# Performance work log

Measured on AMD Instinct MI355X. Metric: run time of the kernel, lower is better.

The kernel has to match this reference:

```python
import jax, jax.numpy as jnp
import numpy as np

N_NODES = 50000
N_EDGES = 1600000
D = 64


def setup_inputs() -> dict:
    key = jax.random.key(0)
    ks = jax.random.split(key, 7)
    scale = 1.0 / np.sqrt(2 * D)  # keep activations sane through relu stack
    x = jax.random.normal(ks[0], (N_NODES, D), dtype=jnp.float32)
    edge_index = jax.random.randint(ks[1], (2, N_EDGES), 0, N_NODES, dtype=jnp.int32)
    edge_weight = jax.random.uniform(ks[2], (N_EDGES,), dtype=jnp.float32)
    W1 = jax.random.normal(ks[3], (D, 2 * D), dtype=jnp.float32) * scale
    b1 = jax.random.normal(ks[4], (D,), dtype=jnp.float32) * 0.01
    W2 = jax.random.normal(ks[5], (D, 2 * D), dtype=jnp.float32) * scale
    b2 = jax.random.normal(ks[6], (D,), dtype=jnp.float32) * 0.01
    return {"x": x, "edge_index": edge_index, "edge_weight": edge_weight,
            "W1": W1, "b1": b1, "W2": W2, "b2": b2}


def _sage_conv(x, src, dst, edge_weight, W, b):
    # gather neighbor features, weight, scatter-mean onto src nodes
    m = x[dst] * edge_weight[:, None]                      # [E, d]
    agg_sum = jax.ops.segment_sum(m, src, num_segments=x.shape[0])
    cnt = jax.ops.segment_sum(jnp.ones_like(edge_weight), src,
                              num_segments=x.shape[0])
    agg = agg_sum / jnp.maximum(cnt, 1.0)[:, None]          # scatter 'mean'
    h = jnp.concatenate([x, agg], axis=1)                   # [N, 2d]
    return h @ W.T + b


def reference(x, edge_index, edge_weight, W1, b1, W2, b2):
    src, dst = edge_index[0], edge_index[1]
    h = jax.nn.relu(_sage_conv(x, src, dst, edge_weight, W1, b1))
    h = jax.nn.relu(_sage_conv(h, src, dst, edge_weight, W2, b2))
    return h
```

## Files before the change

kernel.cpp:

```cpp
#include <hip/hip_runtime.h>

#define NN 50000
#define NE 1600000
#define DD 64
#define NPB 196
#define NBKT 256
#define CHUNK 2500
#define NBLK 640
#define SLOT 24
#define S1CAP 1024
#define SPCAP 512
#define CSRCAP 8192

typedef __attribute__((ext_vector_type(8))) short bf16x8;
typedef __attribute__((ext_vector_type(4))) float f32x4;
typedef __attribute__((ext_vector_type(2))) float f32x2;

static __device__ __forceinline__ unsigned short f2bf(float f) {
    unsigned int u = __float_as_uint(f);
    unsigned int r = (u + 0x7FFFu + ((u >> 16) & 1u)) >> 16;
    return (unsigned short)r;
}
static __device__ __forceinline__ float bf2f(unsigned short h) {
    return __uint_as_float((unsigned int)h << 16);
}
static __device__ __forceinline__ unsigned int pk_fp8x4(float a, float b, float c, float d) {
    unsigned int p = __builtin_amdgcn_cvt_pk_fp8_f32(a, b, 0u, false);
    p = __builtin_amdgcn_cvt_pk_fp8_f32(c, d, p, true);
    return p;
}

__global__ __launch_bounds__(256) void prep(
    const float* __restrict__ x, ushort* __restrict__ xb,
    unsigned int* __restrict__ xf8,
    const float* __restrict__ W1, const float* __restrict__ W2,
    ushort* __restrict__ W1b, ushort* __restrict__ W2b,
    int* __restrict__ gcur)
{
    int b = blockIdx.x, tid = threadIdx.x;
    if (b < 3125) {
        int i = b * 256 + tid;
        float4 v = ((const float4*)x)[i];
        ushort4 o;
        o.x = f2bf(v.x); o.y = f2bf(v.y); o.z = f2bf(v.z); o.w = f2bf(v.w);
        ((ushort4*)xb)[i] = o;
        xf8[i] = pk_fp8x4(v.x, v.y, v.z, v.w);
    } else if (b < 3141) {
        int i = (b - 3125) * 256 + tid;
        const float* src = (i < 2048) ? W1 : W2;
        ushort* dst = (i < 2048) ? W1b : W2b;
        int j = i & 2047;
        float4 v = ((const float4*)src)[j];
        ushort4 o;
        o.x = f2bf(v.x); o.y = f2bf(v.y); o.z = f2bf(v.z); o.w = f2bf(v.w);
        ((ushort4*)dst)[j] = o;
    } else {
        for (int i = tid; i < 2304; i += 256) gcur[i] = 0;
    }
}

__global__ __launch_bounds__(256) void bin_lds(
    const int* __restrict__ ei, const float* __restrict__ ew,
    int* __restrict__ gcur, int* __restrict__ gspillc,
    int2* __restrict__ buf1, int2* __restrict__ spill)
{
    __shared__ int2 slot[NBKT * SLOT];
    __shared__ int  lcnt[NBKT];
    __shared__ int  lbase[NBKT];
    int tid = threadIdx.x;
    int shard = blockIdx.x & 7;

    for (int b = tid; b < NBKT; b += 256) lcnt[b] = 0;
    __syncthreads();

    int e0 = blockIdx.x * CHUNK;
    for (int i = tid; i < CHUNK; i += 256) {
        int e = e0 + i;
        int s = ei[e];
        int d = ei[NE + e];
        float w = ew[e];
        int bkt = s / NPB;
        int sloc = s - bkt * NPB;
        int2 rec = make_int2(d | ((int)f2bf(w) << 16), sloc);
        int pos = atomicAdd(&lcnt[bkt], 1);
        if (pos < SLOT) {
            slot[bkt * SLOT + pos] = rec;
        } else {
            int sp = atomicAdd(&gspillc[bkt], 1);
            if (sp < SPCAP) spill[bkt * SPCAP + sp] = rec;
        }
    }
    __syncthreads();

    {
        int b = tid;
        int n = lcnt[b]; if (n > SLOT) n = SLOT;
        lcnt[b] = n;
        lbase[b] = (n > 0) ? atomicAdd(&gcur[b * 8 + shard], n) : 0;
    }
    __syncthreads();

    int wave = tid >> 6, lane = tid & 63;
    int b0 = wave * 64;
    int vcnt = lcnt[b0 + lane];
    int vbase = lbase[b0 + lane];
#pragma unroll 8
    for (int j = 0; j < 64; ++j) {
        int n = __shfl(vcnt, j);
        int base = __shfl(vbase, j);
        int b = b0 + j;
        if (lane < n) {
            int2 rec = slot[b * SLOT + lane];
            int p = base + lane;
            if (p < S1CAP) {
                buf1[((size_t)b * 8 + shard) * S1CAP + p] = rec;
            } else {
                int sp = atomicAdd(&gspillc[b], 1);
                if (sp < SPCAP) spill[b * SPCAP + sp] = rec;
            }
        }
    }
}

__global__ __launch_bounds__(1024) void build_csr(
    const int* __restrict__ gcur, const int2* __restrict__ buf1,
    const int* __restrict__ gspillc, const int2* __restrict__ spill,
    unsigned int* __restrict__ csr, int* __restrict__ rstart,
    int* __restrict__ cnt)
{
    __shared__ int lcnt[NPB];
    __shared__ int lstart[NPB];
    __shared__ int sa[256], sb[256];
    int tid = threadIdx.x, bkt = blockIdx.x;

    if (tid < NPB) lcnt[tid] = 0;
    __syncthreads();

    for (int sh = 0; sh < 9; ++sh) {
        int n; const int2* rp;
        if (sh < 8) {
            n = gcur[bkt * 8 + sh]; if (n > S1CAP) n = S1CAP;
            rp = buf1 + ((size_t)bkt * 8 + sh) * S1CAP;
        } else {
            n = gspillc[bkt]; if (n > SPCAP) n = SPCAP;
            rp = spill + (size_t)bkt * SPCAP;
        }
        for (int i = tid; i < n; i += 1024)
            atomicAdd(&lcnt[rp[i].y], 1);
    }
    __syncthreads();

    if (tid < 256) sa[tid] = (tid < NPB) ? ((lcnt[tid] + 3) & ~3) : 0;
    __syncthreads();
    int* s = sa; int* d = sb;
    for (int off = 1; off < 256; off <<= 1) {
        if (tid < 256) d[tid] = s[tid] + (tid >= off ? s[tid - off] : 0);
        __syncthreads();
        int* t = s; s = d; d = t;
    }
    if (tid < NPB) {
        int ex = (tid == 0) ? 0 : s[tid - 1];
        lstart[tid] = ex;
        int node = bkt * NPB + tid;
        if (node < NN) {
            rstart[node] = bkt * CSRCAP + ex;
            cnt[node] = lcnt[tid];
        }
    }
    __syncthreads();
    if (tid < NPB) lcnt[tid] = 0;
    __syncthreads();

    for (int sh = 0; sh < 9; ++sh) {
        int n; const int2* rp;
        if (sh < 8) {
            n = gcur[bkt * 8 + sh]; if (n > S1CAP) n = S1CAP;
            rp = buf1 + ((size_t)bkt * 8 + sh) * S1CAP;
        } else {
            n = gspillc[bkt]; if (n > SPCAP) n = SPCAP;
            rp = spill + (size_t)bkt * SPCAP;
        }
        for (int i = tid; i < n; i += 1024) {
            int2 r = rp[i];
            int pos = atomicAdd(&lcnt[r.y], 1);
            csr[bkt * CSRCAP + lstart[r.y] + pos] = (unsigned int)r.x;
        }
    }
    __syncthreads();

    if (tid < NPB) {
        int c = lcnt[tid];
        int c4 = (c + 3) & ~3;
        for (int p = c; p < c4; ++p)
            csr[bkt * CSRCAP + lstart[tid] + p] = 0u;
    }
}

__global__ __launch_bounds__(256) void aggregate(
    const unsigned int* __restrict__ f8,
    const int* __restrict__ rstart, const int* __restrict__ cnt,
    const unsigned int* __restrict__ csr, ushort* __restrict__ aggb)
{
    int node = (blockIdx.x * 256 + threadIdx.x) >> 6;
    int lane = threadIdx.x & 63;
    int g = lane >> 4, l16 = lane & 15;
    int n = cnt[node];
    int n4 = (n + 3) & ~3;
    const unsigned int* __restrict__ rp = csr + rstart[node];
    float a0 = 0.f, a1 = 0.f, a2 = 0.f, a3 = 0.f;

    int i = 0;
    for (; i + 16 <= n4; i += 16) {
        uint4 r = *(const uint4*)(rp + i + g * 4);
        unsigned int v0 = f8[(r.x & 0xFFFF) * 16 + l16];
        unsigned int v1 = f8[(r.y & 0xFFFF) * 16 + l16];
        unsigned int v2 = f8[(r.z & 0xFFFF) * 16 + l16];
        unsigned int v3 = f8[(r.w & 0xFFFF) * 16 + l16];
        float w0 = bf2f((unsigned short)(r.x >> 16));
        float w1 = bf2f((unsigned short)(r.y >> 16));
        float w2 = bf2f((unsigned short)(r.z >> 16));
        float w3 = bf2f((unsigned short)(r.w >> 16));
        f32x2 lo, hi;
        lo = __builtin_amdgcn_cvt_pk_f32_fp8(v0, false);
        hi = __builtin_amdgcn_cvt_pk_f32_fp8(v0, true);
        a0 += w0 * lo.x; a1 += w0 * lo.y; a2 += w0 * hi.x; a3 += w0 * hi.y;
        lo = __builtin_amdgcn_cvt_pk_f32_fp8(v1, false);
        hi = __builtin_amdgcn_cvt_pk_f32_fp8(v1, true);
        a0 += w1 * lo.x; a1 += w1 * lo.y; a2 += w1 * hi.x; a3 += w1 * hi.y;
        lo = __builtin_amdgcn_cvt_pk_f32_fp8(v2, false);
        hi = __builtin_amdgcn_cvt_pk_f32_fp8(v2, true);
        a0 += w2 * lo.x; a1 += w2 * lo.y; a2 += w2 * hi.x; a3 += w2 * hi.y;
        lo = __builtin_amdgcn_cvt_pk_f32_fp8(v3, false);
        hi = __builtin_amdgcn_cvt_pk_f32_fp8(v3, true);
        a0 += w3 * lo.x; a1 += w3 * lo.y; a2 += w3 * hi.x; a3 += w3 * hi.y;
    }
    for (; i < n4; i += 4) {
        uint4 r = *(const uint4*)(rp + i);
        unsigned int e = (g == 0) ? r.x : (g == 1) ? r.y : (g == 2) ? r.z : r.w;
        unsigned int v = f8[(e & 0xFFFF) * 16 + l16];
        float w = bf2f((unsigned short)(e >> 16));
        f32x2 lo = __builtin_amdgcn_cvt_pk_f32_fp8(v, false);
        f32x2 hi = __builtin_amdgcn_cvt_pk_f32_fp8(v, true);
        a0 += w * lo.x; a1 += w * lo.y; a2 += w * hi.x; a3 += w * hi.y;
    }

    a0 += __shfl_xor(a0, 16); a0 += __shfl_xor(a0, 32);
    a1 += __shfl_xor(a1, 16); a1 += __shfl_xor(a1, 32);
    a2 += __shfl_xor(a2, 16); a2 += __shfl_xor(a2, 32);
    a3 += __shfl_xor(a3, 16); a3 += __shfl_xor(a3, 32);

    if (lane < 16) {
        float dm = (float)(n > 1 ? n : 1);
        ushort4 o;
        o.x = f2bf(a0 / dm); o.y = f2bf(a1 / dm);
        o.z = f2bf(a2 / dm); o.w = f2bf(a3 / dm);
        *(ushort4*)&aggb[(size_t)node * DD + l16 * 4] = o;
    }
}

__global__ __launch_bounds__(256) void sage_gemm_mfma(
    const ushort* __restrict__ X, const ushort* __restrict__ A,
    const ushort* __restrict__ Wb, const float* __restrict__ bias,
    float* __restrict__ out, ushort* __restrict__ outb,
    unsigned char* __restrict__ outf8)
{
    int tid = threadIdx.x;
    int wave = tid >> 6, lane = tid & 63;
    int quad = lane >> 4, l16 = lane & 15;
    int m0 = blockIdx.x * 64 + wave * 16;

    int arow = m0 + l16; if (arow >= NN) arow = NN - 1;
    const ushort* __restrict__ ax = X + (size_t)arow * DD;
    const ushort* __restrict__ aa = A + (size_t)arow * DD;

    f32x4 acc[4];
#pragma unroll
    for (int t = 0; t < 4; ++t) acc[t] = (f32x4){0.f, 0.f, 0.f, 0.f};

#pragma unroll
    for (int ki = 0; ki < 4; ++ki) {
        const ushort* ap = (ki < 2) ? (ax + ki * 32 + quad * 8)
                                    : (aa + (ki - 2) * 32 + quad * 8);
        bf16x8 af = *(const bf16x8*)ap;
#pragma unroll
        for (int t = 0; t < 4; ++t) {
            const ushort* bp = Wb + (size_t)(t * 16 + l16) * 128 + ki * 32 + quad * 8;
            bf16x8 bfrag = *(const bf16x8*)bp;
            acc[t] = __builtin_amdgcn_mfma_f32_16x16x32_bf16(af, bfrag, acc[t], 0, 0, 0);
        }
    }

#pragma unroll
    for (int t = 0; t < 4; ++t) {
        int col = t * 16 + l16;
        float bv = bias[col];
#pragma unroll
        for (int r = 0; r < 4; ++r) {
            int grow = m0 + quad * 4 + r;
            if (grow < NN) {
                float v = fmaxf(acc[t][r] + bv, 0.f);
                if (out)  out[(size_t)grow * DD + col] = v;
                if (outb) outb[(size_t)grow * DD + col] = f2bf(v);
                if (outf8) {
                    unsigned int p = __builtin_amdgcn_cvt_pk_fp8_f32(v, v, 0u, false);
                    outf8[(size_t)grow * DD + col] = (unsigned char)(p & 0xFFu);
                }
            }
        }
    }
}

extern "C" void kernel_launch(void* const* d_in, const int* in_sizes, int n_in,
                              void* d_out, int out_size, void* d_ws, size_t ws_size,
                              hipStream_t stream)
{
    const float* x  = (const float*)d_in[0];
    const int*   ei = (const int*)d_in[1];
    const float* ew = (const float*)d_in[2];
    const float* W1 = (const float*)d_in[3];
    const float* b1 = (const float*)d_in[4];
    const float* W2 = (const float*)d_in[5];
    const float* b2 = (const float*)d_in[6];
    float* out = (float*)d_out;

    char* ws = (char*)d_ws;
    int*          gcur    = (int*)ws;
    int*          gspillc = (int*)(ws + 8192);
    int2*         buf1    = (int2*)(ws + 16384);
    int2*         spill   = (int2*)(ws + 16793600);
    unsigned int* csr     = (unsigned int*)(ws + 17842176);
    int*          rstart  = (int*)(ws + 26230784);
    int*          cnt     = (int*)(ws + 26431488);
    ushort*       xb      = (ushort*)(ws + 26632192);
    ushort*       aggb    = (ushort*)(ws + 33032192);
    ushort*       h1b     = (ushort*)(ws + 39432192);
    ushort*       W1b     = (ushort*)(ws + 45832192);
    ushort*       W2b     = (ushort*)(ws + 45848576);
    unsigned int* xf8     = (unsigned int*)(ws + 45864960);
    unsigned char* h1f8   = (unsigned char*)(ws + 49064960);

    prep<<<3142, 256, 0, stream>>>(x, xb, xf8, W1, W2, W1b, W2b, gcur);
    bin_lds<<<NBLK, 256, 0, stream>>>(ei, ew, gcur, gspillc, buf1, spill);
    build_csr<<<NBKT, 1024, 0, stream>>>(gcur, buf1, gspillc, spill, csr, rstart, cnt);

    aggregate<<<(NN * 64) / 256, 256, 0, stream>>>(xf8, rstart, cnt, csr, aggb);
    sage_gemm_mfma<<<(NN + 63) / 64, 256, 0, stream>>>(xb, aggb, W1b, b1, nullptr, h1b, h1f8);

    aggregate<<<(NN * 64) / 256, 256, 0, stream>>>((const unsigned int*)h1f8, rstart, cnt, csr, aggb);
    sage_gemm_mfma<<<(NN + 63) / 64, 256, 0, stream>>>(h1b, aggb, W2b, b2, out, nullptr, nullptr);
}
```

Measured before the change: 202.9 us.

## Pad CSR rows to 16, pack rowstart/count, and shrink binning chunks

Each node's CSR row is now padded to a multiple of 16 entries, so the aggregate loop always runs full 16-edge iterations and the 4-edge tail loop is removed. The row start and count are packed into one int2 array, so each node needs one load instead of two. Binning switches to more blocks with smaller chunks and smaller slots, and CSRCAP grows to hold the extra padding. The cost is extra zero-weight edge work (up to 15 per node) and a larger CSR footprint, which could overflow capacity on skewed inputs.

```diff
diff --git a/kernel.cpp b/kernel.cpp
--- a/kernel.cpp
+++ b/kernel.cpp
@@ -5,12 +5,12 @@
 #define DD 64
 #define NPB 196
 #define NBKT 256
-#define CHUNK 2500
-#define NBLK 640
-#define SLOT 24
+#define CHUNK 1250
+#define NBLK 1280
+#define SLOT 16
 #define S1CAP 1024
 #define SPCAP 512
-#define CSRCAP 8192
+#define CSRCAP 9216
 
 typedef __attribute__((ext_vector_type(8))) short bf16x8;
 typedef __attribute__((ext_vector_type(4))) float f32x4;
@@ -125,8 +125,7 @@
 __global__ __launch_bounds__(1024) void build_csr(
     const int* __restrict__ gcur, const int2* __restrict__ buf1,
     const int* __restrict__ gspillc, const int2* __restrict__ spill,
-    unsigned int* __restrict__ csr, int* __restrict__ rstart,
-    int* __restrict__ cnt)
+    unsigned int* __restrict__ csr, int2* __restrict__ rc)
 {
     __shared__ int lcnt[NPB];
     __shared__ int lstart[NPB];
@@ -150,7 +149,7 @@
     }
     __syncthreads();
 
-    if (tid < 256) sa[tid] = (tid < NPB) ? ((lcnt[tid] + 3) & ~3) : 0;
+    if (tid < 256) sa[tid] = (tid < NPB) ? ((lcnt[tid] + 15) & ~15) : 0;
     __syncthreads();
     int* s = sa; int* d = sb;
     for (int off = 1; off < 256; off <<= 1) {
@@ -162,10 +161,8 @@
         int ex = (tid == 0) ? 0 : s[tid - 1];
         lstart[tid] = ex;
         int node = bkt * NPB + tid;
-        if (node < NN) {
-            rstart[node] = bkt * CSRCAP + ex;
-            cnt[node] = lcnt[tid];
-        }
+        if (node < NN)
+            rc[node] = make_int2(bkt * CSRCAP + ex, lcnt[tid]);
     }
     __syncthreads();
     if (tid < NPB) lcnt[tid] = 0;
@@ -190,27 +187,27 @@
 
     if (tid < NPB) {
         int c = lcnt[tid];
-        int c4 = (c + 3) & ~3;
-        for (int p = c; p < c4; ++p)
+        int c16 = (c + 15) & ~15;
+        for (int p = c; p < c16; ++p)
             csr[bkt * CSRCAP + lstart[tid] + p] = 0u;
     }
 }
 
 __global__ __launch_bounds__(256) void aggregate(
     const unsigned int* __restrict__ f8,
-    const int* __restrict__ rstart, const int* __restrict__ cnt,
-    const unsigned int* __restrict__ csr, ushort* __restrict__ aggb)
+    const int2* __restrict__ rc, const unsigned int* __restrict__ csr,
+    ushort* __restrict__ aggb)
 {
     int node = (blockIdx.x * 256 + threadIdx.x) >> 6;
     int lane = threadIdx.x & 63;
     int g = lane >> 4, l16 = lane & 15;
-    int n = cnt[node];
-    int n4 = (n + 3) & ~3;
-    const unsigned int* __restrict__ rp = csr + rstart[node];
+    int2 rcv = rc[node];
+    int n = rcv.y;
+    int n16 = (n + 15) & ~15;
+    const unsigned int* __restrict__ rp = csr + rcv.x;
     float a0 = 0.f, a1 = 0.f, a2 = 0.f, a3 = 0.f;
 
-    int i = 0;
-    for (; i + 16 <= n4; i += 16) {
+    for (int i = 0; i < n16; i += 16) {
         uint4 r = *(const uint4*)(rp + i + g * 4);
         unsigned int v0 = f8[(r.x & 0xFFFF) * 16 + l16];
         unsigned int v1 = f8[(r.y & 0xFFFF) * 16 + l16];
@@ -234,15 +231,6 @@
         hi = __builtin_amdgcn_cvt_pk_f32_fp8(v3, true);
         a0 += w3 * lo.x; a1 += w3 * lo.y; a2 += w3 * hi.x; a3 += w3 * hi.y;
     }
-    for (; i < n4; i += 4) {
-        uint4 r = *(const uint4*)(rp + i);
-        unsigned int e = (g == 0) ? r.x : (g == 1) ? r.y : (g == 2) ? r.z : r.w;
-        unsigned int v = f8[(e & 0xFFFF) * 16 + l16];
-        float w = bf2f((unsigned short)(e >> 16));
-        f32x2 lo = __builtin_amdgcn_cvt_pk_f32_fp8(v, false);
-        f32x2 hi = __builtin_amdgcn_cvt_pk_f32_fp8(v, true);
-        a0 += w * lo.x; a1 += w * lo.y; a2 += w * hi.x; a3 += w * hi.y;
-    }
 
     a0 += __shfl_xor(a0, 16); a0 += __shfl_xor(a0, 32);
     a1 += __shfl_xor(a1, 16); a1 += __shfl_xor(a1, 32);
@@ -329,23 +317,22 @@
     int2*         buf1    = (int2*)(ws + 16384);
     int2*         spill   = (int2*)(ws + 16793600);
     unsigned int* csr     = (unsigned int*)(ws + 17842176);
-    int*          rstart  = (int*)(ws + 26230784);
-    int*          cnt     = (int*)(ws + 26431488);
-    ushort*       xb      = (ushort*)(ws + 26632192);
-    ushort*       aggb    = (ushort*)(ws + 33032192);
-    ushort*       h1b     = (ushort*)(ws + 39432192);
-    ushort*       W1b     = (ushort*)(ws + 45832192);
-    ushort*       W2b     = (ushort*)(ws + 45848576);
-    unsigned int* xf8     = (unsigned int*)(ws + 45864960);
-    unsigned char* h1f8   = (unsigned char*)(ws + 49064960);
+    int2*         rc      = (int2*)(ws + 27279360);
+    ushort*       xb      = (ushort*)(ws + 27680768);
+    ushort*       aggb    = (ushort*)(ws + 34080768);
+    ushort*       h1b     = (ushort*)(ws + 40480768);
+    ushort*       W1b     = (ushort*)(ws + 46880768);
+    ushort*       W2b     = (ushort*)(ws + 46897152);
+    unsigned int* xf8     = (unsigned int*)(ws + 46913536);
+    unsigned char* h1f8   = (unsigned char*)(ws + 50113536);
 
     prep<<<3142, 256, 0, stream>>>(x, xb, xf8, W1, W2, W1b, W2b, gcur);
     bin_lds<<<NBLK, 256, 0, stream>>>(ei, ew, gcur, gspillc, buf1, spill);
-    build_csr<<<NBKT, 1024, 0, stream>>>(gcur, buf1, gspillc, spill, csr, rstart, cnt);
-
-    aggregate<<<(NN * 64) / 256, 256, 0, stream>>>(xf8, rstart, cnt, csr, aggb);
+    build_csr<<<NBKT, 1024, 0, stream>>>(gcur, buf1, gspillc, spill, csr, rc);
+
+    aggregate<<<(NN * 64) / 256, 256, 0, stream>>>(xf8, rc, csr, aggb);
     sage_gemm_mfma<<<(NN + 63) / 64, 256, 0, stream>>>(xb, aggb, W1b, b1, nullptr, h1b, h1f8);
 
-    aggregate<<<(NN * 64) / 256, 256, 0, stream>>>((const unsigned int*)h1f8, rstart, cnt, csr, aggb);
+    aggregate<<<(NN * 64) / 256, 256, 0, stream>>>((const unsigned int*)h1f8, rc, csr, aggb);
     sage_gemm_mfma<<<(NN + 63) / 64, 256, 0, stream>>>(h1b, aggb, W2b, b2, out, nullptr, nullptr);
 }
```

After: 211.7 us. +4.4%, slower.
